# Kernel tuning notes

Measured on AMD Instinct MI355X. Metric: run time of the kernel, lower is better.

## Reference

```python
import jax, jax.numpy as jnp
import numpy as np

D_MODEL = 1024
N_HEADS = 16
HEAD_DIM = D_MODEL // N_HEADS


def setup_inputs() -> dict:
    key = jax.random.key(0)
    ks = jax.random.split(key, 5)
    scale = 1.0 / np.sqrt(D_MODEL)
    return {
        "x": jax.random.normal(ks[0], (4, 2048, D_MODEL), dtype=jnp.float32),
        "W_q": jax.random.normal(ks[1], (D_MODEL, D_MODEL), dtype=jnp.float32) * scale,
        "W_k": jax.random.normal(ks[2], (D_MODEL, D_MODEL), dtype=jnp.float32) * scale,
        "W_v": jax.random.normal(ks[3], (D_MODEL, D_MODEL), dtype=jnp.float32) * scale,
        "W_o": jax.random.normal(ks[4], (D_MODEL, D_MODEL), dtype=jnp.float32) * scale,
    }


def _split_heads(t):
    # (B, T, d_model) -> (B, H, T, head_dim)
    B, T, _ = t.shape
    return t.reshape(B, T, N_HEADS, HEAD_DIM).transpose(0, 2, 1, 3)


def reference(x, W_q, W_k, W_v, W_o):
    B, T, _ = x.shape
    # torch nn.Linear: y = x @ W.T
    q = _split_heads(x @ W_q.T)
    k = _split_heads(x @ W_k.T)
    v = _split_heads(x @ W_v.T)
    scale = jnp.asarray(np.sqrt(HEAD_DIM), x.dtype)
    # (B, H, T, T) scores, additive causal mask (triu above diagonal = -inf)
    scores = jnp.einsum("bhqd,bhkd->bhqk", q, k) / scale
    causal = jnp.tril(jnp.ones((T, T), dtype=bool))
    scores = jnp.where(causal, scores, jnp.asarray(-jnp.inf, scores.dtype))
    weights = jax.nn.softmax(scores, axis=-1)
    out = jnp.einsum("bhqk,bhkd->bhqd", weights, v)
    out = out.transpose(0, 2, 1, 3).reshape(B, T, D_MODEL)
    out = out @ W_o.T
    return out, k, v
```

## Files before the change

kernel.cpp:

```cpp
#include <hip/hip_runtime.h>
#include <stdint.h>

typedef __bf16 bf16;
typedef __bf16 bf16x8 __attribute__((ext_vector_type(8)));
typedef __bf16 bf16x4 __attribute__((ext_vector_type(4)));
typedef short short4v __attribute__((ext_vector_type(4)));
typedef float f32x4 __attribute__((ext_vector_type(4)));
typedef int v2i __attribute__((ext_vector_type(2)));
typedef uint32_t u32;

#define MFMA_BF16(a, b, c) __builtin_amdgcn_mfma_f32_16x16x32_bf16(a, b, c, 0, 0, 0)
#define MFMA16(a, b, c)                                                   \
  __builtin_amdgcn_mfma_f32_16x16x16bf16_1k(*(const short4v*)&(a),        \
                                            *(const short4v*)&(b), c, 0, 0, 0)

#define TRREAD(dst, va, IMM)                                             \
  asm volatile("ds_read_b64_tr_b16 %0, %1 offset:" #IMM                  \
               : "=v"(dst)                                               \
               : "v"(va))

constexpr int D_MODEL = 1024;
constexpr int T_SEQ = 2048;
constexpr int NH = 16;
constexpr int HD = 64;
constexpr size_t OUT_ELEMS = (size_t)4 * T_SEQ * D_MODEL;
constexpr size_t X_ELEMS = OUT_ELEMS;
constexpr size_t W_ELEMS = (size_t)D_MODEL * D_MODEL;

__device__ __forceinline__ void gload16(const bf16* g, bf16* l) {
  __builtin_amdgcn_global_load_lds(
      (const __attribute__((address_space(1))) unsigned int*)g,
      (__attribute__((address_space(3))) unsigned int*)l, 16, 0, 0);
}

__global__ __launch_bounds__(256) void convert_kernel(
    const float* __restrict__ x, const float* __restrict__ wq,
    const float* __restrict__ wk, const float* __restrict__ wv,
    bf16* __restrict__ dst) {
  const size_t nchunk = (X_ELEMS + 3 * W_ELEMS) / 8;
  for (size_t c = (size_t)blockIdx.x * 256 + threadIdx.x; c < nchunk;
       c += (size_t)gridDim.x * 256) {
    const size_t off = c * 8;
    const float* src;
    size_t rel;
    if (off < X_ELEMS) {
      src = x;
      rel = off;
    } else {
      const size_t j = off - X_ELEMS;
      const int w = (int)(j >> 20);
      rel = j & (W_ELEMS - 1);
      src = (w == 0) ? wq : (w == 1) ? wk : wv;
    }
    const f32x4 a = *(const f32x4*)(src + rel);
    const f32x4 b = *(const f32x4*)(src + rel + 4);
    bf16x8 o;
#pragma unroll
    for (int e = 0; e < 4; ++e) {
      o[e] = (bf16)a[e];
      o[e + 4] = (bf16)b[e];
    }
    *(bf16x8*)(dst + off) = o;
  }
}

__global__ __launch_bounds__(256) void convert_wo(const float* __restrict__ wo,
                                                  bf16* __restrict__ dst) {
  const size_t nchunk = W_ELEMS / 8;
  for (size_t c = (size_t)blockIdx.x * 256 + threadIdx.x; c < nchunk;
       c += (size_t)gridDim.x * 256) {
    const size_t off = c * 8;
    const f32x4 a = *(const f32x4*)(wo + off);
    const f32x4 b = *(const f32x4*)(wo + off + 4);
    bf16x8 o;
#pragma unroll
    for (int e = 0; e < 4; ++e) {
      o[e] = (bf16)a[e];
      o[e + 4] = (bf16)b[e];
    }
    *(bf16x8*)(dst + off) = o;
  }
}

template <bool B_F32>
__global__ __launch_bounds__(256) void gemm2(
    const bf16* __restrict__ A, const bf16* __restrict__ WB,
    const float* __restrict__ WF, int modeBase, bf16* __restrict__ dstB,
    float* __restrict__ dstF1, float* __restrict__ dstF2) {
  const int z = blockIdx.z;
  const int mode = modeBase + z;
  const bf16* Bb = B_F32 ? nullptr : WB + (size_t)z * W_ELEMS;
  const int m0 = blockIdx.y * 128, n0 = blockIdx.x * 128;
  const int tid = threadIdx.x;
  const int wave = tid >> 6, lane = tid & 63;
  const int quad = lane >> 4, c16 = lane & 15;
  const int wr = wave >> 1, wc = wave & 1;

  __shared__ __align__(16) bf16 As[128 * 32];
  __shared__ __align__(16) bf16 Bs[128 * 32];

  f32x4 acc[4][4];
#pragma unroll
  for (int i = 0; i < 4; ++i)
#pragma unroll
    for (int j = 0; j < 4; ++j) acc[i][j] = (f32x4){0.f, 0.f, 0.f, 0.f};

  const int rIn = lane >> 2;
  const int kgo = (lane & 3) * 8;
  const int rA0 = wave * 16 + rIn;
  const int rA1 = (wave + 4) * 16 + rIn;

  for (int k0 = 0; k0 < 1024; k0 += 32) {
    __syncthreads();
    gload16(A + (size_t)(m0 + rA0) * 1024 + k0 + kgo, &As[wave * 512]);
    gload16(A + (size_t)(m0 + rA1) * 1024 + k0 + kgo, &As[(wave + 4) * 512]);
    if (!B_F32) {
      gload16(Bb + (size_t)(n0 + rA0) * 1024 + k0 + kgo, &Bs[wave * 512]);
      gload16(Bb + (size_t)(n0 + rA1) * 1024 + k0 + kgo, &Bs[(wave + 4) * 512]);
    } else {
#pragma unroll
      for (int p = 0; p < 2; ++p) {
        const int slot = p * 256 + tid;
        const int row = slot >> 2, kg = slot & 3;
        const float* bp = WF + (size_t)(n0 + row) * 1024 + k0 + kg * 8;
        const f32x4 b0 = *(const f32x4*)bp;
        const f32x4 b1 = *(const f32x4*)(bp + 4);
        bf16x8 vb;
#pragma unroll
        for (int e = 0; e < 4; ++e) {
          vb[e] = (bf16)b0[e];
          vb[e + 4] = (bf16)b1[e];
        }
        *(bf16x8*)&Bs[(size_t)slot * 8] = vb;
      }
    }
    asm volatile("s_waitcnt vmcnt(0)" ::: "memory");
    __syncthreads();

    const bf16x8* Av = (const bf16x8*)As;
    const bf16x8* Bv = (const bf16x8*)Bs;
    bf16x8 af[4], bfr[4];
#pragma unroll
    for (int i = 0; i < 4; ++i) af[i] = Av[(wr * 64 + i * 16 + c16) * 4 + quad];
#pragma unroll
    for (int j = 0; j < 4; ++j) bfr[j] = Bv[(wc * 64 + j * 16 + c16) * 4 + quad];
#pragma unroll
    for (int i = 0; i < 4; ++i)
#pragma unroll
      for (int j = 0; j < 4; ++j) acc[i][j] = MFMA_BF16(af[i], bfr[j], acc[i][j]);
  }

  const int row0 = m0 + wr * 64, col0 = n0 + wc * 64;
#pragma unroll
  for (int i = 0; i < 4; ++i) {
#pragma unroll
    for (int r = 0; r < 4; ++r) {
      const int row = row0 + i * 16 + quad * 4 + r;
      const int b = row >> 11, t = row & 2047;
#pragma unroll
      for (int j = 0; j < 4; ++j) {
        const int cc = col0 + j * 16 + c16;
        const float v = acc[i][j][r];
        if (mode == 0) {
          dstB[(size_t)row * 1024 + cc] = (bf16)v;
        } else if (mode == 3) {
          dstF1[(size_t)row * 1024 + cc] = v;
        } else {
          const int h = cc >> 6, d = cc & 63;
          float* df = (mode == 1) ? dstF1 : dstF2;
          df[((size_t)(b * NH + h) * T_SEQ + t) * HD + d] = v;
        }
      }
    }
  }
}

__device__ __forceinline__ void load_kv(const float* Kg, const float* Vg,
                                        int t0, int st, int sd,
                                        f32x4 pk[2][2], f32x4 pv[2][2]) {
#pragma unroll
  for (int p = 0; p < 2; ++p) {
    const float* kp = Kg + (size_t)(t0 + p * 32 + st) * HD + sd * 8;
    pk[p][0] = *(const f32x4*)kp;
    pk[p][1] = *(const f32x4*)(kp + 4);
    const float* vp = Vg + (size_t)(t0 + p * 32 + st) * HD + sd * 8;
    pv[p][0] = *(const f32x4*)vp;
    pv[p][1] = *(const f32x4*)(vp + 4);
  }
}

__global__ __launch_bounds__(256, 4) void attn_kernel(
    const bf16* __restrict__ Q, const float* __restrict__ K,
    const float* __restrict__ V, bf16* __restrict__ Aout) {
  const int bx = blockIdx.x;
  const int by = blockIdx.y;
  const int r16 = (bx + ((by >> 4) << 2)) & 15;
  const int qt = (r16 < 8) ? r16 : 23 - r16;
  const int b = by >> 4, h = by & 15;
  const int tid = threadIdx.x, wave = tid >> 6, lane = tid & 63;
  const int quad = lane >> 4, c16 = lane & 15;

  __shared__ __align__(16) bf16 Ks[64 * 70];
  __shared__ __align__(16) bf16 Vs[4096];

  const int q0w = qt * 128 + wave * 32;
  const bf16* Qb = Q + ((size_t)b * T_SEQ + q0w) * D_MODEL + h * HD;
  const float* Kg = K + (size_t)by * T_SEQ * HD;
  const float* Vg = V + (size_t)by * T_SEQ * HD;

  bf16x8 aq[2][2];
#pragma unroll
  for (int mt = 0; mt < 2; ++mt) {
    const bf16* qp = Qb + (size_t)(mt * 16 + c16) * D_MODEL + quad * 8;
    aq[mt][0] = *(const bf16x8*)qp;
    aq[mt][1] = *(const bf16x8*)(qp + 32);
  }

  f32x4 O[2][4], racc[2];
#pragma unroll
  for (int mt = 0; mt < 2; ++mt) {
    racc[mt] = (f32x4){0.f, 0.f, 0.f, 0.f};
#pragma unroll
    for (int dj = 0; dj < 4; ++dj) O[mt][dj] = (f32x4){0.f, 0.f, 0.f, 0.f};
  }

  bf16x4 ones4;
#pragma unroll
  for (int e = 0; e < 4; ++e) ones4[e] = (bf16)1.0f;

  const float sc = 0.125f * 1.44269504088896340736f;
  const int nkt = 2 * qt + 2;
  const int st = tid >> 3, sd = tid & 7;
  const u32 vtr =
      (u32)(uintptr_t)(const __attribute__((address_space(3))) bf16*)Vs +
      (u32)lane * 8;

  f32x4 pk[2][2], pv[2][2];
  load_kv(Kg, Vg, 0, st, sd, pk, pv);

  for (int kt = 0; kt < nkt; ++kt) {
    const int t0 = kt * 64;

    __syncthreads();
#pragma unroll
    for (int p = 0; p < 2; ++p) {
      const int t = p * 32 + st;
      bf16x8 kb, vb;
#pragma unroll
      for (int e = 0; e < 4; ++e) {
        kb[e] = (bf16)pk[p][0][e];
        kb[e + 4] = (bf16)pk[p][1][e];
        vb[e] = (bf16)pv[p][0][e];
        vb[e + 4] = (bf16)pv[p][1][e];
      }
      *(bf16x8*)&Ks[t * 70 + sd * 8] = kb;
      *(bf16x8*)&Vs[(((t >> 4) * 4 + (sd >> 1)) * 256) + (t & 15) * 16 +
                    (sd & 1) * 8] = vb;
    }
    if (kt + 1 < nkt) load_kv(Kg, Vg, t0 + 64, st, sd, pk, pv);
    __syncthreads();

    const bool act[2] = {t0 <= q0w + 15, t0 <= q0w + 31};

    bf16x4 ap16[2][4];
#pragma unroll
    for (int j = 0; j < 4; ++j) {
      const bf16* kp = &Ks[(j * 16 + c16) * 70 + quad * 8];
      const bf16x8 ak0 = *(const bf16x8*)kp;
      const bf16x8 ak1 = *(const bf16x8*)(kp + 32);
#pragma unroll
      for (int mt = 0; mt < 2; ++mt) {
        if (!act[mt]) continue;
        f32x4 s = (f32x4){0.f, 0.f, 0.f, 0.f};
        s = MFMA_BF16(ak0, aq[mt][0], s);
        s = MFMA_BF16(ak1, aq[mt][1], s);
        const int trow = t0 + j * 16 + quad * 4;
        const int qcol = q0w + mt * 16 + c16;
        bf16x4 pa;
#pragma unroll
        for (int r = 0; r < 4; ++r)
          pa[r] = (bf16)((trow + r <= qcol) ? exp2f(s[r] * sc) : 0.f);
        ap16[mt][j] = pa;
      }
    }

    if (act[1]) {
#pragma unroll
      for (int mt = 0; mt < 2; ++mt) {
        if (!act[mt]) continue;
#pragma unroll
        for (int j = 0; j < 4; ++j)
          racc[mt] = MFMA16(ap16[mt][j], ones4, racc[mt]);
      }
      v2i bv0, bv1, bv2, bv3;
#define PV_DJ(DJ, O0, O1, O2, O3)                                        \
  {                                                                      \
    TRREAD(bv0, vtr, O0);                                                \
    TRREAD(bv1, vtr, O1);                                                \
    TRREAD(bv2, vtr, O2);                                                \
    TRREAD(bv3, vtr, O3);                                                \
    asm volatile("s_waitcnt lgkmcnt(0)" ::: "memory");                   \
    __builtin_amdgcn_sched_barrier(0);                                   \
    _Pragma("unroll") for (int mt = 0; mt < 2; ++mt) {                   \
      if (act[mt]) {                                                     \
        O[mt][DJ] = MFMA16(ap16[mt][0], bv0, O[mt][DJ]);                 \
        O[mt][DJ] = MFMA16(ap16[mt][1], bv1, O[mt][DJ]);                 \
        O[mt][DJ] = MFMA16(ap16[mt][2], bv2, O[mt][DJ]);                 \
        O[mt][DJ] = MFMA16(ap16[mt][3], bv3, O[mt][DJ]);                 \
      }                                                                  \
    }                                                                    \
  }
      PV_DJ(0, 0, 2048, 4096, 6144)
      PV_DJ(1, 512, 2560, 4608, 6656)
      PV_DJ(2, 1024, 3072, 5120, 7168)
      PV_DJ(3, 1536, 3584, 5632, 7680)
#undef PV_DJ
    }
  }

#pragma unroll
  for (int mt = 0; mt < 2; ++mt) {
    f32x4 inv;
#pragma unroll
    for (int r = 0; r < 4; ++r) inv[r] = 1.f / racc[mt][r];
#pragma unroll
    for (int dj = 0; dj < 4; ++dj)
#pragma unroll
      for (int r = 0; r < 4; ++r) {
        const int q = q0w + mt * 16 + quad * 4 + r;
        Aout[((size_t)b * T_SEQ + q) * D_MODEL + h * HD + dj * 16 + c16] =
            (bf16)(O[mt][dj][r] * inv[r]);
      }
  }
}

extern "C" void kernel_launch(void* const* d_in, const int* in_sizes, int n_in,
                              void* d_out, int out_size, void* d_ws, size_t ws_size,
                              hipStream_t stream) {
  const float* x = (const float*)d_in[0];
  const float* wq = (const float*)d_in[1];
  const float* wk = (const float*)d_in[2];
  const float* wv = (const float*)d_in[3];
  const float* wo = (const float*)d_in[4];

  float* out = (float*)d_out;
  float* kout = out + OUT_ELEMS;
  float* vout = out + 2 * OUT_ELEMS;

  bf16* ws = (bf16*)d_ws;
  bf16* Qbuf = ws;
  bf16* Abuf = ws;

  bf16* cvt = (bf16*)d_out;
  const bf16* xb = cvt;
  const bf16* wb = cvt + X_ELEMS;

  const bool wo_bf = ws_size >= (X_ELEMS + W_ELEMS) * sizeof(bf16);
  bf16* wo_b = ws + X_ELEMS;

  convert_kernel<<<dim3(2048), 256, 0, stream>>>(x, wq, wk, wv, cvt);
  if (wo_bf) convert_wo<<<dim3(512), 256, 0, stream>>>(wo, wo_b);
  gemm2<false><<<dim3(8, 64, 3), 256, 0, stream>>>(xb, wb, nullptr, 0, Qbuf,
                                                   kout, vout);
  attn_kernel<<<dim3(16, 64), 256, 0, stream>>>(Qbuf, kout, vout, Abuf);
  if (wo_bf) {
    gemm2<false><<<dim3(8, 64, 1), 256, 0, stream>>>(Abuf, wo_b, nullptr, 3,
                                                     nullptr, out, nullptr);
  } else {
    gemm2<true><<<dim3(8, 64, 1), 256, 0, stream>>>(Abuf, nullptr, wo, 3,
                                                    nullptr, out, nullptr);
  }
}
```

Baseline: 388.8 us.

## Double GEMM K-tile to 64 with XOR-swizzled LDS and merge weight conversions

The GEMM now loads a 64-wide K slice per iteration instead of 32 and stores it in LDS with an XOR swizzle, reading it with a matching swizzle. This halves the number of barrier and wait cycles per output tile and avoids bank conflicts on the wider rows. The separate W_o conversion kernel is folded into the main conversion kernel, which removes one launch. The cost is twice the LDS per block, which may lower occupancy.

```diff
diff --git a/kernel.cpp b/kernel.cpp
--- a/kernel.cpp
+++ b/kernel.cpp
@@ -36,21 +36,31 @@
 __global__ __launch_bounds__(256) void convert_kernel(
     const float* __restrict__ x, const float* __restrict__ wq,
     const float* __restrict__ wk, const float* __restrict__ wv,
-    bf16* __restrict__ dst) {
-  const size_t nchunk = (X_ELEMS + 3 * W_ELEMS) / 8;
+    const float* __restrict__ wo, bf16* __restrict__ dst,
+    bf16* __restrict__ wo_b) {
+  const size_t nchunk = (X_ELEMS + 4 * W_ELEMS) / 8;
   for (size_t c = (size_t)blockIdx.x * 256 + threadIdx.x; c < nchunk;
        c += (size_t)gridDim.x * 256) {
     const size_t off = c * 8;
     const float* src;
+    bf16* d;
     size_t rel;
     if (off < X_ELEMS) {
       src = x;
       rel = off;
+      d = dst + off;
     } else {
       const size_t j = off - X_ELEMS;
       const int w = (int)(j >> 20);
       rel = j & (W_ELEMS - 1);
-      src = (w == 0) ? wq : (w == 1) ? wk : wv;
+      if (w == 3) {
+        if (!wo_b) continue;
+        src = wo;
+        d = wo_b + rel;
+      } else {
+        src = (w == 0) ? wq : (w == 1) ? wk : wv;
+        d = dst + off;
+      }
     }
     const f32x4 a = *(const f32x4*)(src + rel);
     const f32x4 b = *(const f32x4*)(src + rel + 4);
@@ -60,25 +70,7 @@
       o[e] = (bf16)a[e];
       o[e + 4] = (bf16)b[e];
     }
-    *(bf16x8*)(dst + off) = o;
-  }
-}
-
-__global__ __launch_bounds__(256) void convert_wo(const float* __restrict__ wo,
-                                                  bf16* __restrict__ dst) {
-  const size_t nchunk = W_ELEMS / 8;
-  for (size_t c = (size_t)blockIdx.x * 256 + threadIdx.x; c < nchunk;
-       c += (size_t)gridDim.x * 256) {
-    const size_t off = c * 8;
-    const f32x4 a = *(const f32x4*)(wo + off);
-    const f32x4 b = *(const f32x4*)(wo + off + 4);
-    bf16x8 o;
-#pragma unroll
-    for (int e = 0; e < 4; ++e) {
-      o[e] = (bf16)a[e];
-      o[e + 4] = (bf16)b[e];
-    }
-    *(bf16x8*)(dst + off) = o;
+    *(bf16x8*)d = o;
   }
 }
 
@@ -96,8 +88,8 @@
   const int quad = lane >> 4, c16 = lane & 15;
   const int wr = wave >> 1, wc = wave & 1;
 
-  __shared__ __align__(16) bf16 As[128 * 32];
-  __shared__ __align__(16) bf16 Bs[128 * 32];
+  __shared__ __align__(16) bf16 As[128 * 64];
+  __shared__ __align__(16) bf16 Bs[128 * 64];
 
   f32x4 acc[4][4];
 #pragma unroll
@@ -105,24 +97,27 @@
 #pragma unroll
     for (int j = 0; j < 4; ++j) acc[i][j] = (f32x4){0.f, 0.f, 0.f, 0.f};
 
-  const int rIn = lane >> 2;
-  const int kgo = (lane & 3) * 8;
-  const int rA0 = wave * 16 + rIn;
-  const int rA1 = (wave + 4) * 16 + rIn;
-
-  for (int k0 = 0; k0 < 1024; k0 += 32) {
+  const int r8 = lane >> 3;
+  const int s8 = lane & 7;
+  const int ksw = ((s8 ^ r8) * 8);
+  const int swA = (c16 & 7);
+
+  for (int k0 = 0; k0 < 1024; k0 += 64) {
     __syncthreads();
-    gload16(A + (size_t)(m0 + rA0) * 1024 + k0 + kgo, &As[wave * 512]);
-    gload16(A + (size_t)(m0 + rA1) * 1024 + k0 + kgo, &As[(wave + 4) * 512]);
-    if (!B_F32) {
-      gload16(Bb + (size_t)(n0 + rA0) * 1024 + k0 + kgo, &Bs[wave * 512]);
-      gload16(Bb + (size_t)(n0 + rA1) * 1024 + k0 + kgo, &Bs[(wave + 4) * 512]);
-    } else {
-#pragma unroll
-      for (int p = 0; p < 2; ++p) {
-        const int slot = p * 256 + tid;
-        const int row = slot >> 2, kg = slot & 3;
-        const float* bp = WF + (size_t)(n0 + row) * 1024 + k0 + kg * 8;
+#pragma unroll
+    for (int c = 0; c < 4; ++c) {
+      const int chunk = wave + c * 4;
+      const int row = chunk * 8 + r8;
+      gload16(A + (size_t)(m0 + row) * 1024 + k0 + ksw, &As[chunk * 512]);
+      if (!B_F32)
+        gload16(Bb + (size_t)(n0 + row) * 1024 + k0 + ksw, &Bs[chunk * 512]);
+    }
+    if (B_F32) {
+#pragma unroll
+      for (int g = 0; g < 4; ++g) {
+        const int gi = g * 256 + tid;
+        const int row = gi >> 3, s = gi & 7;
+        const float* bp = WF + (size_t)(n0 + row) * 1024 + k0 + s * 8;
         const f32x4 b0 = *(const f32x4*)bp;
         const f32x4 b1 = *(const f32x4*)(bp + 4);
         bf16x8 vb;
@@ -131,23 +126,31 @@
           vb[e] = (bf16)b0[e];
           vb[e + 4] = (bf16)b1[e];
         }
-        *(bf16x8*)&Bs[(size_t)slot * 8] = vb;
+        *(bf16x8*)&Bs[row * 64 + ((s ^ (row & 7)) * 8)] = vb;
       }
     }
     asm volatile("s_waitcnt vmcnt(0)" ::: "memory");
     __syncthreads();
 
-    const bf16x8* Av = (const bf16x8*)As;
-    const bf16x8* Bv = (const bf16x8*)Bs;
-    bf16x8 af[4], bfr[4];
-#pragma unroll
-    for (int i = 0; i < 4; ++i) af[i] = Av[(wr * 64 + i * 16 + c16) * 4 + quad];
-#pragma unroll
-    for (int j = 0; j < 4; ++j) bfr[j] = Bv[(wc * 64 + j * 16 + c16) * 4 + quad];
-#pragma unroll
-    for (int i = 0; i < 4; ++i)
-#pragma unroll
-      for (int j = 0; j < 4; ++j) acc[i][j] = MFMA_BF16(af[i], bfr[j], acc[i][j]);
+#pragma unroll
+    for (int kk = 0; kk < 2; ++kk) {
+      bf16x8 af[4], bfr[4];
+#pragma unroll
+      for (int i = 0; i < 4; ++i) {
+        const int row = wr * 64 + i * 16 + c16;
+        af[i] = *(const bf16x8*)&As[row * 64 + (((quad + kk * 4) ^ swA) * 8)];
+      }
+#pragma unroll
+      for (int j = 0; j < 4; ++j) {
+        const int row = wc * 64 + j * 16 + c16;
+        bfr[j] = *(const bf16x8*)&Bs[row * 64 + (((quad + kk * 4) ^ swA) * 8)];
+      }
+#pragma unroll
+      for (int i = 0; i < 4; ++i)
+#pragma unroll
+        for (int j = 0; j < 4; ++j)
+          acc[i][j] = MFMA_BF16(af[i], bfr[j], acc[i][j]);
+    }
   }
 
   const int row0 = m0 + wr * 64, col0 = n0 + wc * 64;
@@ -356,10 +359,9 @@
   const bf16* wb = cvt + X_ELEMS;
 
   const bool wo_bf = ws_size >= (X_ELEMS + W_ELEMS) * sizeof(bf16);
-  bf16* wo_b = ws + X_ELEMS;
-
-  convert_kernel<<<dim3(2048), 256, 0, stream>>>(x, wq, wk, wv, cvt);
-  if (wo_bf) convert_wo<<<dim3(512), 256, 0, stream>>>(wo, wo_b);
+  bf16* wo_b = wo_bf ? (ws + X_ELEMS) : nullptr;
+
+  convert_kernel<<<dim3(2048), 256, 0, stream>>>(x, wq, wk, wv, wo, cvt, wo_b);
   gemm2<false><<<dim3(8, 64, 3), 256, 0, stream>>>(xb, wb, nullptr, 0, Qbuf,
                                                    kout, vout);
   attn_kernel<<<dim3(16, 64), 256, 0, stream>>>(Qbuf, kout, vout, Abuf);
```

Result: faster. 377.0 us (median of 2 runs) (-3.0%).
